# Optimization experiments

Hardware: AMD Instinct MI355X
Metric: run time of the kernel (lower is better)

Reference implementation:

```python
import jax, jax.numpy as jnp
import numpy as np

B, S, D = 2, 2048, 1024
H, DH = 16, 64  # n_heads, d_head = d_model // n_heads


def setup_inputs() -> dict:
    key = jax.random.key(0)
    ks = jax.random.split(key, 8)
    sc = lambda d: 1.0 / np.sqrt(d)
    return {
        "x": jax.random.normal(ks[0], (B, S, D), jnp.float32),
        "context": jax.random.normal(ks[1], (B, D), jnp.float32),
        "prev_state": jax.random.normal(ks[2], (B, S, D), jnp.float32),
        "attention_mask": jnp.ones((B, 1, S, S), dtype=bool),
        "Wq": jax.random.normal(ks[3], (D, D), jnp.float32) * sc(D),
        "Wk": jax.random.normal(ks[4], (D, D), jnp.float32) * sc(D),
        "Wv": jax.random.normal(ks[5], (D, D), jnp.float32) * sc(D),
        "Wo": jax.random.normal(ks[6], (D, D), jnp.float32) * sc(D),
        "Wc": jax.random.normal(ks[7], (D, DH), jnp.float32) * sc(D),
        "alpha": jnp.ones((1,), jnp.float32),
        "beta": jnp.ones((1,), jnp.float32),
    }


def reference(x, context, prev_state, attention_mask, Wq, Wk, Wv, Wo, Wc, alpha, beta):
    b, s, d = x.shape
    # projections (Linear with no bias, weight stored as [out, in] -> x @ W.T)
    q = (x @ Wq.T).reshape(b, s, H, DH).transpose(0, 2, 1, 3)  # (B,H,S,DH)
    k = (x @ Wk.T).reshape(b, s, H, DH).transpose(0, 2, 1, 3)
    v = (x @ Wv.T).reshape(b, s, H, DH).transpose(0, 2, 1, 3)

    inv_sqrt_dh = 1.0 / jnp.sqrt(jnp.asarray(DH, x.dtype))
    scores = jnp.einsum("bhqd,bhkd->bhqk", q, k) * inv_sqrt_dh

    # CFM: context-flow matching bias, rank-1 per-pair term from global context
    c = context @ Wc  # (B, DH)
    qc = jnp.einsum("bhqd,bd->bhq", q, c)
    kc = jnp.einsum("bhkd,bd->bhk", k, c)
    cfm = qc[..., :, None] * kc[..., None, :] / DH  # (B,H,S,S)

    # AFM: anti-flow matching bias from previous layer state (first d_head dims)
    p = prev_state[..., :DH]  # (B,S,DH)
    afm = jnp.einsum("bhqd,bkd->bhqk", q, p) * inv_sqrt_dh

    scores = scores + alpha[0] * cfm - beta[0] * afm
    scores = jnp.where(attention_mask, scores, jnp.asarray(-1e9, scores.dtype))

    w = jax.nn.softmax(scores, axis=-1)
    out = jnp.einsum("bhqk,bhkd->bhqd", w, v)  # (B,H,S,DH)
    out = out.transpose(0, 2, 1, 3).reshape(b, s, d)
    return out @ Wo.T
```

## Files before the change

kernel.cpp:

```cpp
#include <hip/hip_runtime.h>
#include <stdint.h>

#define D_  1024
#define S_  2048
#define B_  2
#define H_  16
#define DH_ 64
#define M_  (B_*S_)

typedef __bf16 bf16x8 __attribute__((ext_vector_type(8)));
typedef float  f32x4  __attribute__((ext_vector_type(4)));
typedef float  f32x16 __attribute__((ext_vector_type(16)));
typedef short  short8 __attribute__((ext_vector_type(8)));
typedef unsigned uint4v __attribute__((ext_vector_type(4)));
typedef unsigned short u16;

static __device__ __forceinline__ u16 f2bf(float f){
  union { float f; unsigned u; } v; v.f = f;
  unsigned r = v.u + 0x7FFF + ((v.u >> 16) & 1);
  return (u16)(r >> 16);
}
static __device__ __forceinline__ f32x4 mfma16(short8 a, short8 b, f32x4 c){
  return __builtin_amdgcn_mfma_f32_16x16x32_bf16(
      __builtin_bit_cast(bf16x8, a), __builtin_bit_cast(bf16x8, b), c, 0, 0, 0);
}
static __device__ __forceinline__ f32x16 mfma32(short8 a, short8 b, f32x16 c){
  return __builtin_amdgcn_mfma_f32_32x32x16_bf16(
      __builtin_bit_cast(bf16x8, a), __builtin_bit_cast(bf16x8, b), c, 0, 0, 0);
}
static __device__ __forceinline__ f32x16 zero16(){
  f32x16 z = {0,0,0,0,0,0,0,0,0,0,0,0,0,0,0,0};
  return z;
}
static __device__ __forceinline__ float fexp2(float x){
#if __has_builtin(__builtin_amdgcn_exp2f)
  return __builtin_amdgcn_exp2f(x);
#else
  return __exp2f(x);
#endif
}
static __device__ __forceinline__ unsigned cvtpk(float lo, float hi){
  unsigned r;
  asm("v_cvt_pk_bf16_f32 %0, %1, %2" : "=v"(r) : "v"(lo), "v"(hi));
  return r;
}
static __device__ __forceinline__ void gl_lds16(const u16* g, u16* lds){
  __builtin_amdgcn_global_load_lds(
      (const __attribute__((address_space(1))) void*)(uintptr_t)g,
      (__attribute__((address_space(3))) void*)(uintptr_t)lds, 16, 0, 0);
}

__global__ void k_f2bf(const float* __restrict__ in, u16* __restrict__ out, int n4){
  int i = blockIdx.x * blockDim.x + threadIdx.x;
  if(i >= n4) return;
  float4 v = ((const float4*)in)[i];
  ushort4 o; o.x = f2bf(v.x); o.y = f2bf(v.y); o.z = f2bf(v.z); o.w = f2bf(v.w);
  ((ushort4*)out)[i] = o;
}

__global__ void k_f2bf4(const float* __restrict__ a0, const float* __restrict__ a1,
                        const float* __restrict__ a2, const float* __restrict__ a3,
                        u16* __restrict__ o0, u16* __restrict__ o1,
                        u16* __restrict__ o2, u16* __restrict__ o3, int n4){
  const float* in; u16* out;
  switch(blockIdx.y){
    case 0: in=a0; out=o0; break;
    case 1: in=a1; out=o1; break;
    case 2: in=a2; out=o2; break;
    default: in=a3; out=o3; break;
  }
  int i = blockIdx.x * blockDim.x + threadIdx.x;
  if(i >= n4) return;
  float4 v = ((const float4*)in)[i];
  ushort4 o; o.x = f2bf(v.x); o.y = f2bf(v.y); o.z = f2bf(v.z); o.w = f2bf(v.w);
  ((ushort4*)out)[i] = o;
}

__global__ void k_ctx(const float* __restrict__ context, const float* __restrict__ Wc,
                      float* __restrict__ cvec, int* __restrict__ flags){
  __shared__ float partial[4][2][64];
  int t = threadIdx.x;
  if(t < 2) flags[t] = 1;
  int c = t >> 7;
  int b = (t >> 6) & 1;
  int j = t & 63;
  float s = 0.f;
  #pragma unroll 8
  for(int d = c*256; d < (c+1)*256; ++d) s += context[b*D_ + d] * Wc[d*DH_ + j];
  partial[c][b][j] = s;
  __syncthreads();
  if(t < 128){
    int b2 = t >> 6, j2 = t & 63;
    cvec[b2*DH_ + j2] = partial[0][b2][j2] + partial[1][b2][j2]
                      + partial[2][b2][j2] + partial[3][b2][j2];
  }
}

__global__ void k_mask_check(const uint4* __restrict__ m, int n16, int* flags){
  int i = blockIdx.x * blockDim.x + threadIdx.x;
  bool ok8 = true, ok32 = true;
  if(i < n16){
    uint4 v = m[i];
    ok8  = (v.x==0x01010101u)&&(v.y==0x01010101u)&&(v.z==0x01010101u)&&(v.w==0x01010101u);
    ok32 = (v.x==1u)&&(v.y==1u)&&(v.z==1u)&&(v.w==1u);
  }
  unsigned long long b8  = __ballot(!ok8);
  unsigned long long b32 = __ballot(!ok32);
  if((threadIdx.x & 63) == 0){
    if(b8)  flags[0] = 0;
    if(b32) flags[1] = 0;
  }
}

template<int MODE>
__global__ __launch_bounds__(256,2) void k_gemm(const u16* __restrict__ A, const u16* __restrict__ W,
                                                void* __restrict__ Cout,
                                                const float* __restrict__ cvec,
                                                const float* __restrict__ prev,
                                                const float* __restrict__ beta_p,
                                                float* __restrict__ qkc){
  __shared__ u16 As[128*64];
  __shared__ u16 Bs[64*64];
  __shared__ float red[2][2][64];
  const int tid = threadIdx.x;
  const int w = tid >> 6, l = tid & 63;
  const int wr = w >> 1, wc = w & 1;
  const int bm = blockIdx.x >> 4;
  const int bn = blockIdx.x & 15;
  const int lr = l & 15, lh = l >> 4;
  const int srow = l >> 3, scol = (l & 7) * 8;

  f32x4 acc[4][2] = {};

  for(int kt = 0; kt < 16; ++kt){
    const int k0 = kt * 64;
    #pragma unroll
    for(int i = 0; i < 4; ++i){
      const int chunk = i*4 + w;
      const u16* ga = A + (size_t)(bm*128 + chunk*8 + srow)*D_ + k0 + scol;
      gl_lds16(ga, &As[chunk*512]);
    }
    #pragma unroll
    for(int i = 0; i < 2; ++i){
      const int chunk = w*2 + i;
      const u16* gb = W + (size_t)(bn*64 + chunk*8 + srow)*D_ + k0 + scol;
      gl_lds16(gb, &Bs[chunk*512]);
    }
    __syncthreads();
    #pragma unroll
    for(int kk = 0; kk < 2; ++kk){
      short8 a[4], b[2];
      #pragma unroll
      for(int m = 0; m < 4; ++m)
        a[m] = *(const short8*)&As[(wr*64 + m*16 + lr)*64 + kk*32 + lh*8];
      #pragma unroll
      for(int n = 0; n < 2; ++n)
        b[n] = *(const short8*)&Bs[(wc*32 + n*16 + lr)*64 + kk*32 + lh*8];
      #pragma unroll
      for(int m = 0; m < 4; ++m)
        #pragma unroll
        for(int n = 0; n < 2; ++n)
          acc[m][n] = mfma16(a[m], b[n], acc[m][n]);
    }
    __syncthreads();
  }

  const int b = bm >> 4;

  if constexpr (MODE <= 1){
    const float cv0 = cvec[b*DH_ + wc*32 + lr];
    const float cv1 = cvec[b*DH_ + wc*32 + 16 + lr];
    float part[4][4];
    #pragma unroll
    for(int m = 0; m < 4; ++m)
      #pragma unroll
      for(int r = 0; r < 4; ++r){
        float p = acc[m][0][r]*cv0 + acc[m][1][r]*cv1;
        p += __shfl_xor(p, 1, 64); p += __shfl_xor(p, 2, 64);
        p += __shfl_xor(p, 4, 64); p += __shfl_xor(p, 8, 64);
        part[m][r] = p;
      }
    if(lr == 0){
      #pragma unroll
      for(int m = 0; m < 4; ++m)
        #pragma unroll
        for(int r = 0; r < 4; ++r)
          red[wr][wc][m*16 + lh*4 + r] = part[m][r];
    }
    __syncthreads();
    if(tid < 128){
      int wr2 = tid >> 6, i = tid & 63;
      float v = red[wr2][0][i] + red[wr2][1][i];
      int s = (bm & 15)*128 + wr2*64 + i;
      qkc[((size_t)b*H_ + bn)*S_ + s] = v;
    }
  }

  if constexpr (MODE == 1){
    const float beta = beta_p[0];
    const float KSCALE = 0.125f * 1.44269504088896340736f;
    #pragma unroll
    for(int m = 0; m < 4; ++m)
      #pragma unroll
      for(int n = 0; n < 2; ++n)
        #pragma unroll
        for(int r = 0; r < 4; ++r){
          size_t row = (size_t)bm*128 + wr*64 + m*16 + lh*4 + r;
          acc[m][n][r] = (acc[m][n][r] - beta * prev[row*D_ + wc*32 + n*16 + lr]) * KSCALE;
        }
  }

  if constexpr (MODE == 2){
    #pragma unroll
    for(int m = 0; m < 4; ++m){
      const int s0 = (bm & 15)*128 + wr*64 + m*16 + lh*4;
      #pragma unroll
      for(int n = 0; n < 2; ++n){
        const int col = bn*64 + wc*32 + n*16 + lr;
        ushort4 o;
        o.x = f2bf(acc[m][n][0]); o.y = f2bf(acc[m][n][1]);
        o.z = f2bf(acc[m][n][2]); o.w = f2bf(acc[m][n][3]);
        *(ushort4*)&((u16*)Cout)[((size_t)(b*1024 + col))*S_ + s0] = o;
      }
    }
  } else {
    #pragma unroll
    for(int m = 0; m < 4; ++m){
      const size_t row0 = (size_t)bm*128 + wr*64 + m*16 + lh*4;
      #pragma unroll
      for(int n = 0; n < 2; ++n){
        const size_t col = (size_t)bn*64 + wc*32 + n*16 + lr;
        #pragma unroll
        for(int r = 0; r < 4; ++r){
          if constexpr (MODE == 3) ((float*)Cout)[(row0 + r)*D_ + col] = acc[m][n][r];
          else                     ((u16*)Cout)[(row0 + r)*D_ + col] = f2bf(acc[m][n][r]);
        }
      }
    }
  }
}

__global__ __launch_bounds__(128,2) void k_attn(const u16* __restrict__ Qb,
    const u16* __restrict__ Kb, const u16* __restrict__ VT,
    const float* __restrict__ qc, const float* __restrict__ kc,
    const float* __restrict__ alpha_p, const unsigned char* __restrict__ mask,
    const int* __restrict__ flags, u16* __restrict__ Ob){
  __shared__ u16 Kbuf[2][4096];
  __shared__ u16 Vbuf[2][4096];
  const int tid = threadIdx.x;
  const int wv = tid >> 6, l = tid & 63;
  const int q32 = l & 31, hi = l >> 5, hb = hi*8;
  const int id = blockIdx.x;
  const int bh = id & 31, qb = id >> 5;
  const int b = bh >> 4, h = bh & 15;
  const int q0w = qb*64 + wv*32;
  const float aL = alpha_p[0] * (1.0f/64.0f) * 1.44269504088896340736f;
  const bool allones = (flags[0] | flags[1]) != 0;
  const u16* Kb_h = Kb + (size_t)b*S_*D_ + h*DH_;
  const u16* VT_h = VT + ((size_t)(b*1024 + h*DH_))*S_;
  const float* kcp = kc + (size_t)bh*S_;
  const unsigned char* maskr = mask + ((size_t)b*S_ + q0w + q32)*S_;

  const int srow = l >> 3;
  const int sdh  = ((l & 7) ^ srow) * 8;
  #define STAGEK(TILE, BUF) { _Pragma("unroll") for(int j = 0; j < 4; ++j){      \
      const int ck = j*2 + wv;                                                   \
      gl_lds16(Kb_h + (size_t)((TILE)*64 + ck*8 + srow)*D_ + sdh,                \
               &Kbuf[BUF][ck*512]); } }
  #define STAGEV(TILE, BUF) { _Pragma("unroll") for(int j = 0; j < 4; ++j){      \
      const int ck = j*2 + wv;                                                   \
      gl_lds16(VT_h + (size_t)(ck*8 + srow)*S_ + (TILE)*64 + sdh,                \
               &Vbuf[BUF][ck*512]); } }

  short8 qa[4];
  #pragma unroll
  for(int c = 0; c < 4; ++c)
    qa[c] = *(const short8*)&Qb[((size_t)b*S_ + q0w + q32)*D_ + h*DH_ + c*16 + hb];
  const float aq = aL * qc[(size_t)bh*S_ + q0w + q32];

  f32x16 oacc[2] = {zero16(), zero16()};
  float lp = 0.f;
  const int xk = (q32 & 7) << 3;

  STAGEK(0, 0);
  STAGEV(0, 0);
  __syncthreads();

  for(int kt = 0; kt < 32; ++kt){
    const int buf = kt & 1;
    const int k0 = kt*64;
    const int tn = (kt+1) & 31;
    STAGEK(tn, buf^1);
    STAGEV(tn, buf^1);

    f32x16 sacc[2] = {zero16(), zero16()};
    #pragma unroll
    for(int kg = 0; kg < 2; ++kg)
      #pragma unroll
      for(int c = 0; c < 4; ++c){
        short8 kf = *(const short8*)&Kbuf[buf][(kg*32 + q32)*64 + ((c*16 + hb) ^ xk)];
        sacc[kg] = mfma32(kf, qa[c], sacc[kg]);
      }
    short8 vf[2][4];
    #pragma unroll
    for(int dh2 = 0; dh2 < 2; ++dh2)
      #pragma unroll
      for(int c = 0; c < 4; ++c)
        vf[dh2][c] = *(const short8*)&Vbuf[buf][(dh2*32 + q32)*64 + ((c*16 + hb) ^ xk)];

    unsigned pk[2][8];
    #pragma unroll
    for(int kg = 0; kg < 2; ++kg){
      float p[16];
      #pragma unroll
      for(int rg = 0; rg < 4; ++rg){
        f32x4 kv = *(const f32x4*)&kcp[k0 + kg*32 + rg*8 + hi*4];
        unsigned mu = 0x01010101u;
        if(!allones) mu = *(const unsigned*)&maskr[k0 + kg*32 + rg*8 + hi*4];
        #pragma unroll
        for(int j = 0; j < 4; ++j){
          float t = sacc[kg][rg*4 + j] + aq*kv[j];
          if(((mu >> (8*j)) & 255u) == 0u) t = -160.0f;
          float e = fexp2(t);
          lp += e;
          p[rg*4 + j] = e;
        }
      }
      #pragma unroll
      for(int i = 0; i < 8; ++i) pk[kg][i] = cvtpk(p[2*i], p[2*i+1]);
    }

    #pragma unroll
    for(int c = 0; c < 4; ++c){
      const int kg = c >> 1, c4 = (c & 1)*4;
      unsigned x0 = pk[kg][c4+0], y0 = pk[kg][c4+2];
      unsigned x1 = pk[kg][c4+1], y1 = pk[kg][c4+3];
      asm("v_permlane32_swap_b32 %0, %1" : "+v"(x0), "+v"(y0));
      asm("v_permlane32_swap_b32 %0, %1" : "+v"(x1), "+v"(y1));
      uint4v pb = {x0, x1, y0, y1};
      short8 pbf = __builtin_bit_cast(short8, pb);
      #pragma unroll
      for(int dh2 = 0; dh2 < 2; ++dh2)
        oacc[dh2] = mfma32(vf[dh2][c], pbf, oacc[dh2]);
    }
    __syncthreads();
  }
  #undef STAGEK
  #undef STAGEV

  float lt = lp + __shfl_xor(lp, 32, 64);
  float inv = 1.0f / lt;
  u16* orow = Ob + ((size_t)b*S_ + q0w + q32)*D_ + h*DH_;
  #pragma unroll
  for(int dh2 = 0; dh2 < 2; ++dh2)
    #pragma unroll
    for(int rg = 0; rg < 4; ++rg){
      ushort4 o;
      o.x = f2bf(oacc[dh2][rg*4+0]*inv);
      o.y = f2bf(oacc[dh2][rg*4+1]*inv);
      o.z = f2bf(oacc[dh2][rg*4+2]*inv);
      o.w = f2bf(oacc[dh2][rg*4+3]*inv);
      *(ushort4*)&orow[dh2*32 + rg*8 + hi*4] = o;
    }
}

extern "C" void kernel_launch(void* const* d_in, const int* in_sizes, int n_in,
                              void* d_out, int out_size, void* d_ws, size_t ws_size,
                              hipStream_t stream){
  const float* x    = (const float*)d_in[0];
  const float* ctx  = (const float*)d_in[1];
  const float* prev = (const float*)d_in[2];
  const unsigned char* mask = (const unsigned char*)d_in[3];
  const float* Wq = (const float*)d_in[4];
  const float* Wk = (const float*)d_in[5];
  const float* Wv = (const float*)d_in[6];
  const float* Wo = (const float*)d_in[7];
  const float* Wc = (const float*)d_in[8];
  const float* alpha = (const float*)d_in[9];
  const float* beta  = (const float*)d_in[10];

  char* ws = (char*)d_ws;
  size_t off = 0;
  auto alloc = [&](size_t bytes)->void*{
    void* p = ws + off; off += (bytes + 255) & ~(size_t)255; return p;
  };
  u16* xb  = (u16*)alloc((size_t)M_*D_*2);
  u16* wqb = (u16*)alloc((size_t)D_*D_*2);
  u16* wkb = (u16*)alloc((size_t)D_*D_*2);
  u16* wvb = (u16*)alloc((size_t)D_*D_*2);
  u16* wob = (u16*)alloc((size_t)D_*D_*2);
  u16* Qb  = (u16*)alloc((size_t)M_*D_*2);
  u16* Kb  = (u16*)alloc((size_t)M_*D_*2);
  u16* VT  = (u16*)alloc((size_t)B_*D_*S_*2);
  float* qcb  = (float*)alloc((size_t)B_*H_*S_*4);
  float* kcb  = (float*)alloc((size_t)B_*H_*S_*4);
  float* cvec = (float*)alloc(512);
  int*  flags = (int*)alloc(64);
  u16* Ob = xb;

  k_f2bf<<<M_*D_/4/256, 256, 0, stream>>>(x, xb, M_*D_/4);
  {
    dim3 g(D_*D_/4/256, 4);
    k_f2bf4<<<g, 256, 0, stream>>>(Wq, Wk, Wv, Wo, wqb, wkb, wvb, wob, D_*D_/4);
  }
  k_ctx<<<1, 512, 0, stream>>>(ctx, Wc, cvec, flags);
  {
    int n16 = B_*S_*S_/16;
    k_mask_check<<<n16/256, 256, 0, stream>>>((const uint4*)mask, n16, flags);
  }
  k_gemm<0><<<512, 256, 0, stream>>>(xb, wqb, Qb, cvec, nullptr, nullptr, qcb);
  k_gemm<1><<<512, 256, 0, stream>>>(xb, wkb, Kb, cvec, prev, beta, kcb);
  k_gemm<2><<<512, 256, 0, stream>>>(xb, wvb, VT, cvec, nullptr, nullptr, nullptr);
  k_attn<<<1024, 128, 0, stream>>>(Qb, Kb, VT, qcb, kcb, alpha, mask, flags, Ob);
  k_gemm<3><<<512, 256, 0, stream>>>(Ob, wob, d_out, cvec, nullptr, nullptr, nullptr);
}
```

Before: 174.2 us.

## Split attention KV range across warps and enlarge GEMM tiles to 128x128

The GEMM kernels move from 128x64 to 128x128 output tiles (256 blocks, launch bounds of 1), which doubles per-wave MFMA work and reuse of the A tile. Attention now uses 256 threads per block, with two warp pairs each covering half the key range; partial outputs and row sums are combined through LDS at the end. V fragments are read straight from global memory instead of being staged in LDS. The all-ones mask path becomes a template specialization. Risks are fewer GEMM blocks on a large GPU (only 256 tiles), uncoalesced or uncached global V reads, and extra LDS reduction cost.

```diff
diff --git a/kernel.cpp b/kernel.cpp
--- a/kernel.cpp
+++ b/kernel.cpp
@@ -113,53 +113,47 @@
 }
 
 template<int MODE>
-__global__ __launch_bounds__(256,2) void k_gemm(const u16* __restrict__ A, const u16* __restrict__ W,
+__global__ __launch_bounds__(256,1) void k_gemm(const u16* __restrict__ A, const u16* __restrict__ W,
                                                 void* __restrict__ Cout,
                                                 const float* __restrict__ cvec,
                                                 const float* __restrict__ prev,
                                                 const float* __restrict__ beta_p,
                                                 float* __restrict__ qkc){
   __shared__ u16 As[128*64];
-  __shared__ u16 Bs[64*64];
+  __shared__ u16 Bs[128*64];
   __shared__ float red[2][2][64];
   const int tid = threadIdx.x;
   const int w = tid >> 6, l = tid & 63;
   const int wr = w >> 1, wc = w & 1;
-  const int bm = blockIdx.x >> 4;
-  const int bn = blockIdx.x & 15;
+  const int bm = blockIdx.x >> 3;
+  const int bn = blockIdx.x & 7;
   const int lr = l & 15, lh = l >> 4;
   const int srow = l >> 3, scol = (l & 7) * 8;
 
-  f32x4 acc[4][2] = {};
+  f32x4 acc[4][4] = {};
 
   for(int kt = 0; kt < 16; ++kt){
     const int k0 = kt * 64;
     #pragma unroll
     for(int i = 0; i < 4; ++i){
       const int chunk = i*4 + w;
-      const u16* ga = A + (size_t)(bm*128 + chunk*8 + srow)*D_ + k0 + scol;
-      gl_lds16(ga, &As[chunk*512]);
-    }
-    #pragma unroll
-    for(int i = 0; i < 2; ++i){
-      const int chunk = w*2 + i;
-      const u16* gb = W + (size_t)(bn*64 + chunk*8 + srow)*D_ + k0 + scol;
-      gl_lds16(gb, &Bs[chunk*512]);
+      gl_lds16(A + (size_t)(bm*128 + chunk*8 + srow)*D_ + k0 + scol, &As[chunk*512]);
+      gl_lds16(W + (size_t)(bn*128 + chunk*8 + srow)*D_ + k0 + scol, &Bs[chunk*512]);
     }
     __syncthreads();
     #pragma unroll
     for(int kk = 0; kk < 2; ++kk){
-      short8 a[4], b[2];
+      short8 a[4], b[4];
       #pragma unroll
       for(int m = 0; m < 4; ++m)
         a[m] = *(const short8*)&As[(wr*64 + m*16 + lr)*64 + kk*32 + lh*8];
       #pragma unroll
-      for(int n = 0; n < 2; ++n)
-        b[n] = *(const short8*)&Bs[(wc*32 + n*16 + lr)*64 + kk*32 + lh*8];
+      for(int n = 0; n < 4; ++n)
+        b[n] = *(const short8*)&Bs[(wc*64 + n*16 + lr)*64 + kk*32 + lh*8];
       #pragma unroll
       for(int m = 0; m < 4; ++m)
         #pragma unroll
-        for(int n = 0; n < 2; ++n)
+        for(int n = 0; n < 4; ++n)
           acc[m][n] = mfma16(a[m], b[n], acc[m][n]);
     }
     __syncthreads();
@@ -168,14 +162,16 @@
   const int b = bm >> 4;
 
   if constexpr (MODE <= 1){
-    const float cv0 = cvec[b*DH_ + wc*32 + lr];
-    const float cv1 = cvec[b*DH_ + wc*32 + 16 + lr];
+    float cv[4];
+    #pragma unroll
+    for(int n = 0; n < 4; ++n) cv[n] = cvec[b*DH_ + n*16 + lr];
     float part[4][4];
     #pragma unroll
     for(int m = 0; m < 4; ++m)
       #pragma unroll
       for(int r = 0; r < 4; ++r){
-        float p = acc[m][0][r]*cv0 + acc[m][1][r]*cv1;
+        float p = acc[m][0][r]*cv[0] + acc[m][1][r]*cv[1]
+                + acc[m][2][r]*cv[2] + acc[m][3][r]*cv[3];
         p += __shfl_xor(p, 1, 64); p += __shfl_xor(p, 2, 64);
         p += __shfl_xor(p, 4, 64); p += __shfl_xor(p, 8, 64);
         part[m][r] = p;
@@ -188,11 +184,10 @@
           red[wr][wc][m*16 + lh*4 + r] = part[m][r];
     }
     __syncthreads();
-    if(tid < 128){
-      int wr2 = tid >> 6, i = tid & 63;
-      float v = red[wr2][0][i] + red[wr2][1][i];
+    {
+      int wr2 = tid >> 7, wc2 = (tid >> 6) & 1, i = tid & 63;
       int s = (bm & 15)*128 + wr2*64 + i;
-      qkc[((size_t)b*H_ + bn)*S_ + s] = v;
+      qkc[((size_t)b*H_ + bn*2 + wc2)*S_ + s] = red[wr2][wc2][i];
     }
   }
 
@@ -202,11 +197,11 @@
     #pragma unroll
     for(int m = 0; m < 4; ++m)
       #pragma unroll
-      for(int n = 0; n < 2; ++n)
+      for(int n = 0; n < 4; ++n)
         #pragma unroll
         for(int r = 0; r < 4; ++r){
           size_t row = (size_t)bm*128 + wr*64 + m*16 + lh*4 + r;
-          acc[m][n][r] = (acc[m][n][r] - beta * prev[row*D_ + wc*32 + n*16 + lr]) * KSCALE;
+          acc[m][n][r] = (acc[m][n][r] - beta * prev[row*D_ + n*16 + lr]) * KSCALE;
         }
   }
 
@@ -215,8 +210,8 @@
     for(int m = 0; m < 4; ++m){
       const int s0 = (bm & 15)*128 + wr*64 + m*16 + lh*4;
       #pragma unroll
-      for(int n = 0; n < 2; ++n){
-        const int col = bn*64 + wc*32 + n*16 + lr;
+      for(int n = 0; n < 4; ++n){
+        const int col = bn*128 + wc*64 + n*16 + lr;
         ushort4 o;
         o.x = f2bf(acc[m][n][0]); o.y = f2bf(acc[m][n][1]);
         o.z = f2bf(acc[m][n][2]); o.w = f2bf(acc[m][n][3]);
@@ -228,8 +223,8 @@
     for(int m = 0; m < 4; ++m){
       const size_t row0 = (size_t)bm*128 + wr*64 + m*16 + lh*4;
       #pragma unroll
-      for(int n = 0; n < 2; ++n){
-        const size_t col = (size_t)bn*64 + wc*32 + n*16 + lr;
+      for(int n = 0; n < 4; ++n){
+        const size_t col = (size_t)bn*128 + wc*64 + n*16 + lr;
         #pragma unroll
         for(int r = 0; r < 4; ++r){
           if constexpr (MODE == 3) ((float*)Cout)[(row0 + r)*D_ + col] = acc[m][n][r];
@@ -240,74 +235,38 @@
   }
 }
 
-__global__ __launch_bounds__(128,2) void k_attn(const u16* __restrict__ Qb,
-    const u16* __restrict__ Kb, const u16* __restrict__ VT,
-    const float* __restrict__ qc, const float* __restrict__ kc,
-    const float* __restrict__ alpha_p, const unsigned char* __restrict__ mask,
-    const int* __restrict__ flags, u16* __restrict__ Ob){
-  __shared__ u16 Kbuf[2][4096];
-  __shared__ u16 Vbuf[2][4096];
-  const int tid = threadIdx.x;
-  const int wv = tid >> 6, l = tid & 63;
-  const int q32 = l & 31, hi = l >> 5, hb = hi*8;
-  const int id = blockIdx.x;
-  const int bh = id & 31, qb = id >> 5;
-  const int b = bh >> 4, h = bh & 15;
-  const int q0w = qb*64 + wv*32;
-  const float aL = alpha_p[0] * (1.0f/64.0f) * 1.44269504088896340736f;
-  const bool allones = (flags[0] | flags[1]) != 0;
-  const u16* Kb_h = Kb + (size_t)b*S_*D_ + h*DH_;
-  const u16* VT_h = VT + ((size_t)(b*1024 + h*DH_))*S_;
-  const float* kcp = kc + (size_t)bh*S_;
-  const unsigned char* maskr = mask + ((size_t)b*S_ + q0w + q32)*S_;
-
-  const int srow = l >> 3;
-  const int sdh  = ((l & 7) ^ srow) * 8;
-  #define STAGEK(TILE, BUF) { _Pragma("unroll") for(int j = 0; j < 4; ++j){      \
-      const int ck = j*2 + wv;                                                   \
-      gl_lds16(Kb_h + (size_t)((TILE)*64 + ck*8 + srow)*D_ + sdh,                \
-               &Kbuf[BUF][ck*512]); } }
-  #define STAGEV(TILE, BUF) { _Pragma("unroll") for(int j = 0; j < 4; ++j){      \
-      const int ck = j*2 + wv;                                                   \
-      gl_lds16(VT_h + (size_t)(ck*8 + srow)*S_ + (TILE)*64 + sdh,                \
-               &Vbuf[BUF][ck*512]); } }
-
-  short8 qa[4];
-  #pragma unroll
-  for(int c = 0; c < 4; ++c)
-    qa[c] = *(const short8*)&Qb[((size_t)b*S_ + q0w + q32)*D_ + h*DH_ + c*16 + hb];
-  const float aq = aL * qc[(size_t)bh*S_ + q0w + q32];
-
-  f32x16 oacc[2] = {zero16(), zero16()};
-  float lp = 0.f;
-  const int xk = (q32 & 7) << 3;
-
-  STAGEK(0, 0);
-  STAGEV(0, 0);
+template<bool AM>
+__device__ __forceinline__ void attn_loop(
+    const u16* __restrict__ Kstream, const u16* __restrict__ VTk,
+    const float* __restrict__ kcp, const unsigned char* __restrict__ maskr,
+    u16* __restrict__ kbuf, const short8 (&qa)[4], float aq,
+    f32x16 (&oacc)[2], float& lp,
+    int q32, int hi, int hb, int srow, int sdh, int stg0, int xk){
+  #define STG(T, BUF) { _Pragma("unroll") for(int j = 0; j < 4; ++j){            \
+      const int ck = stg0 + j;                                                   \
+      gl_lds16(Kstream + (size_t)((T)*64 + ck*8 + srow)*D_ + sdh,                \
+               kbuf + (BUF)*4096 + ck*512); } }
+  STG(0, 0);
   __syncthreads();
-
-  for(int kt = 0; kt < 32; ++kt){
-    const int buf = kt & 1;
-    const int k0 = kt*64;
-    const int tn = (kt+1) & 31;
-    STAGEK(tn, buf^1);
-    STAGEV(tn, buf^1);
-
+  #pragma unroll 2
+  for(int t = 0; t < 16; ++t){
+    const int buf = t & 1;
+    const int k0 = t*64;
+    if(t < 15) STG(t+1, buf^1);
+    short8 vf[2][4];
+    #pragma unroll
+    for(int dh2 = 0; dh2 < 2; ++dh2)
+      #pragma unroll
+      for(int c = 0; c < 4; ++c)
+        vf[dh2][c] = *(const short8*)&VTk[(size_t)(dh2*32 + q32)*S_ + k0 + c*16 + hb];
     f32x16 sacc[2] = {zero16(), zero16()};
     #pragma unroll
     for(int kg = 0; kg < 2; ++kg)
       #pragma unroll
       for(int c = 0; c < 4; ++c){
-        short8 kf = *(const short8*)&Kbuf[buf][(kg*32 + q32)*64 + ((c*16 + hb) ^ xk)];
+        short8 kf = *(const short8*)&kbuf[buf*4096 + (kg*32 + q32)*64 + ((c*16 + hb) ^ xk)];
         sacc[kg] = mfma32(kf, qa[c], sacc[kg]);
       }
-    short8 vf[2][4];
-    #pragma unroll
-    for(int dh2 = 0; dh2 < 2; ++dh2)
-      #pragma unroll
-      for(int c = 0; c < 4; ++c)
-        vf[dh2][c] = *(const short8*)&Vbuf[buf][(dh2*32 + q32)*64 + ((c*16 + hb) ^ xk)];
-
     unsigned pk[2][8];
     #pragma unroll
     for(int kg = 0; kg < 2; ++kg){
@@ -316,12 +275,12 @@
       for(int rg = 0; rg < 4; ++rg){
         f32x4 kv = *(const f32x4*)&kcp[k0 + kg*32 + rg*8 + hi*4];
         unsigned mu = 0x01010101u;
-        if(!allones) mu = *(const unsigned*)&maskr[k0 + kg*32 + rg*8 + hi*4];
+        if(AM) mu = *(const unsigned*)&maskr[k0 + kg*32 + rg*8 + hi*4];
         #pragma unroll
         for(int j = 0; j < 4; ++j){
-          float t = sacc[kg][rg*4 + j] + aq*kv[j];
-          if(((mu >> (8*j)) & 255u) == 0u) t = -160.0f;
-          float e = fexp2(t);
+          float tv = sacc[kg][rg*4 + j] + aq*kv[j];
+          if(AM){ if(((mu >> (8*j)) & 255u) == 0u) tv = -160.0f; }
+          float e = fexp2(tv);
           lp += e;
           p[rg*4 + j] = e;
         }
@@ -329,7 +288,6 @@
       #pragma unroll
       for(int i = 0; i < 8; ++i) pk[kg][i] = cvtpk(p[2*i], p[2*i+1]);
     }
-
     #pragma unroll
     for(int c = 0; c < 4; ++c){
       const int kg = c >> 1, c4 = (c & 1)*4;
@@ -345,23 +303,77 @@
     }
     __syncthreads();
   }
-  #undef STAGEK
-  #undef STAGEV
-
-  float lt = lp + __shfl_xor(lp, 32, 64);
-  float inv = 1.0f / lt;
-  u16* orow = Ob + ((size_t)b*S_ + q0w + q32)*D_ + h*DH_;
+  #undef STG
+}
+
+__global__ __launch_bounds__(256,2) void k_attn(const u16* __restrict__ Qb,
+    const u16* __restrict__ Kb, const u16* __restrict__ VT,
+    const float* __restrict__ qc, const float* __restrict__ kc,
+    const float* __restrict__ alpha_p, const unsigned char* __restrict__ mask,
+    const int* __restrict__ flags, u16* __restrict__ Ob){
+  __shared__ u16 Kbuf[2][2][4096];
+  const int tid = threadIdx.x;
+  const int w = tid >> 6, l = tid & 63;
+  const int qi = w & 1, kh = w >> 1;
+  const int q32 = l & 31, hi = l >> 5, hb = hi*8;
+  const int id = blockIdx.x;
+  const int bh = id & 31, qb = id >> 5;
+  const int b = bh >> 4, h = bh & 15;
+  const int q0w = qb*64 + qi*32;
+  const float aL = alpha_p[0] * (1.0f/64.0f) * 1.44269504088896340736f;
+  const bool allones = (flags[0] | flags[1]) != 0;
+  const u16* Kstream = Kb + (size_t)b*S_*D_ + h*DH_ + (size_t)kh*1024*D_;
+  const u16* VTk = VT + ((size_t)(b*1024 + h*DH_))*S_ + kh*1024;
+  const float* kcp = kc + (size_t)bh*S_ + kh*1024;
+  const unsigned char* maskr = mask + ((size_t)b*S_ + q0w + q32)*S_ + kh*1024;
+  const int srow = l >> 3;
+  const int sdh  = ((l & 7) ^ srow) * 8;
+  const int stg0 = qi*4;
+  const int xk   = (q32 & 7) << 3;
+
+  short8 qa[4];
   #pragma unroll
-  for(int dh2 = 0; dh2 < 2; ++dh2)
-    #pragma unroll
-    for(int rg = 0; rg < 4; ++rg){
-      ushort4 o;
-      o.x = f2bf(oacc[dh2][rg*4+0]*inv);
-      o.y = f2bf(oacc[dh2][rg*4+1]*inv);
-      o.z = f2bf(oacc[dh2][rg*4+2]*inv);
-      o.w = f2bf(oacc[dh2][rg*4+3]*inv);
-      *(ushort4*)&orow[dh2*32 + rg*8 + hi*4] = o;
-    }
+  for(int c = 0; c < 4; ++c)
+    qa[c] = *(const short8*)&Qb[((size_t)b*S_ + q0w + q32)*D_ + h*DH_ + c*16 + hb];
+  const float aq = aL * qc[(size_t)bh*S_ + q0w + q32];
+
+  f32x16 oacc[2] = {zero16(), zero16()};
+  float lp = 0.f;
+
+  if(allones)
+    attn_loop<false>(Kstream, VTk, kcp, maskr, &Kbuf[kh][0][0], qa, aq,
+                     oacc, lp, q32, hi, hb, srow, sdh, stg0, xk);
+  else
+    attn_loop<true>(Kstream, VTk, kcp, maskr, &Kbuf[kh][0][0], qa, aq,
+                    oacc, lp, q32, hi, hb, srow, sdh, stg0, xk);
+
+  float* C = (float*)&Kbuf[0][0][0];
+  float* R = C + qi*2112;
+  if(kh == 1){
+    #pragma unroll
+    for(int i = 0; i < 32; ++i) R[i*64 + l] = oacc[i>>4][i&15];
+    R[2048 + l] = lp;
+  }
+  __syncthreads();
+  if(kh == 0){
+    #pragma unroll
+    for(int i = 0; i < 32; ++i) oacc[i>>4][i&15] += R[i*64 + l];
+    lp += R[2048 + l];
+    float lt = lp + __shfl_xor(lp, 32, 64);
+    float inv = 1.0f / lt;
+    u16* orow = Ob + ((size_t)b*S_ + q0w + q32)*D_ + h*DH_;
+    #pragma unroll
+    for(int dh2 = 0; dh2 < 2; ++dh2)
+      #pragma unroll
+      for(int rg = 0; rg < 4; ++rg){
+        ushort4 o;
+        o.x = f2bf(oacc[dh2][rg*4+0]*inv);
+        o.y = f2bf(oacc[dh2][rg*4+1]*inv);
+        o.z = f2bf(oacc[dh2][rg*4+2]*inv);
+        o.w = f2bf(oacc[dh2][rg*4+3]*inv);
+        *(ushort4*)&orow[dh2*32 + rg*8 + hi*4] = o;
+      }
+  }
 }
 
 extern "C" void kernel_launch(void* const* d_in, const int* in_sizes, int n_in,
@@ -408,9 +420,9 @@
     int n16 = B_*S_*S_/16;
     k_mask_check<<<n16/256, 256, 0, stream>>>((const uint4*)mask, n16, flags);
   }
-  k_gemm<0><<<512, 256, 0, stream>>>(xb, wqb, Qb, cvec, nullptr, nullptr, qcb);
-  k_gemm<1><<<512, 256, 0, stream>>>(xb, wkb, Kb, cvec, prev, beta, kcb);
-  k_gemm<2><<<512, 256, 0, stream>>>(xb, wvb, VT, cvec, nullptr, nullptr, nullptr);
-  k_attn<<<1024, 128, 0, stream>>>(Qb, Kb, VT, qcb, kcb, alpha, mask, flags, Ob);
-  k_gemm<3><<<512, 256, 0, stream>>>(Ob, wob, d_out, cvec, nullptr, nullptr, nullptr);
-}
+  k_gemm<0><<<256, 256, 0, stream>>>(xb, wqb, Qb, cvec, nullptr, nullptr, qcb);
+  k_gemm<1><<<256, 256, 0, stream>>>(xb, wkb, Kb, cvec, prev, beta, kcb);
+  k_gemm<2><<<256, 256, 0, stream>>>(xb, wvb, VT, cvec, nullptr, nullptr, nullptr);
+  k_attn<<<1024, 256, 0, stream>>>(Qb, Kb, VT, qcb, kcb, alpha, mask, flags, Ob);
+  k_gemm<3><<<256, 256, 0, stream>>>(Ob, wob, d_out, cvec, nullptr, nullptr, nullptr);
+}
```

Measured after the change: 229.3 us. 31.7% more time.

## Fuse Q/K/V projections into one GEMM with concatenated weights and wider tiles

Applied to the files above, without the earlier changes.

Concatenates Wq, Wk and Wv into a single bf16 weight buffer and replaces three separate projection GEMM launches with one 768-block kernel using 128x128 output tiles. The per-tile epilogue then branches on column block to write Q plus qc, K plus kc with the prev-state correction, or transposed V. This removes two launches, fills the GPU with a single larger grid, and doubles the B-tile reuse of each A tile. In exchange, each thread holds more accumulator registers, which may reduce occupancy, and the epilogue has divergent per-block paths.

```diff
diff --git a/kernel.cpp b/kernel.cpp
--- a/kernel.cpp
+++ b/kernel.cpp
@@ -112,16 +112,134 @@
   }
 }
 
-template<int MODE>
-__global__ __launch_bounds__(256,2) void k_gemm(const u16* __restrict__ A, const u16* __restrict__ W,
-                                                void* __restrict__ Cout,
-                                                const float* __restrict__ cvec,
-                                                const float* __restrict__ prev,
-                                                const float* __restrict__ beta_p,
-                                                float* __restrict__ qkc){
+__global__ __launch_bounds__(256,2) void k_gemm_qkv(const u16* __restrict__ A,
+    const u16* __restrict__ Wcat, u16* __restrict__ Qb, u16* __restrict__ Kb,
+    u16* __restrict__ VT, const float* __restrict__ cvec,
+    const float* __restrict__ prev, const float* __restrict__ beta_p,
+    float* __restrict__ qcb, float* __restrict__ kcb){
+  __shared__ u16 As[128*64];
+  __shared__ u16 Bs[128*64];
+  __shared__ float red[2][2][64];
+  const int tid = threadIdx.x;
+  const int w = tid >> 6, l = tid & 63;
+  const int wr = w >> 1, wc = w & 1;
+  const int id = blockIdx.x;
+  const int bn = id >> 5;
+  const int bm = id & 31;
+  const int lr = l & 15, lh = l >> 4;
+  const int srow = l >> 3, scol = (l & 7) * 8;
+
+  f32x4 acc[4][4] = {};
+
+  for(int kt = 0; kt < 16; ++kt){
+    const int k0 = kt * 64;
+    #pragma unroll
+    for(int i = 0; i < 4; ++i){
+      const int chunk = i*4 + w;
+      gl_lds16(A    + (size_t)(bm*128 + chunk*8 + srow)*D_ + k0 + scol, &As[chunk*512]);
+      gl_lds16(Wcat + (size_t)(bn*128 + chunk*8 + srow)*D_ + k0 + scol, &Bs[chunk*512]);
+    }
+    __syncthreads();
+    #pragma unroll
+    for(int kk = 0; kk < 2; ++kk){
+      short8 a[4], b[4];
+      #pragma unroll
+      for(int m = 0; m < 4; ++m)
+        a[m] = *(const short8*)&As[(wr*64 + m*16 + lr)*64 + kk*32 + lh*8];
+      #pragma unroll
+      for(int n = 0; n < 4; ++n)
+        b[n] = *(const short8*)&Bs[(wc*64 + n*16 + lr)*64 + kk*32 + lh*8];
+      #pragma unroll
+      for(int m = 0; m < 4; ++m)
+        #pragma unroll
+        for(int n = 0; n < 4; ++n)
+          acc[m][n] = mfma16(a[m], b[n], acc[m][n]);
+    }
+    __syncthreads();
+  }
+
+  const int b = bm >> 4;
+
+  if(bn < 16){
+    float cv[4];
+    #pragma unroll
+    for(int n = 0; n < 4; ++n) cv[n] = cvec[b*DH_ + n*16 + lr];
+    float part[4][4];
+    #pragma unroll
+    for(int m = 0; m < 4; ++m)
+      #pragma unroll
+      for(int r = 0; r < 4; ++r){
+        float p = acc[m][0][r]*cv[0] + acc[m][1][r]*cv[1]
+                + acc[m][2][r]*cv[2] + acc[m][3][r]*cv[3];
+        p += __shfl_xor(p, 1, 64); p += __shfl_xor(p, 2, 64);
+        p += __shfl_xor(p, 4, 64); p += __shfl_xor(p, 8, 64);
+        part[m][r] = p;
+      }
+    if(lr == 0){
+      #pragma unroll
+      for(int m = 0; m < 4; ++m)
+        #pragma unroll
+        for(int r = 0; r < 4; ++r)
+          red[wr][wc][m*16 + lh*4 + r] = part[m][r];
+    }
+    __syncthreads();
+    {
+      int wr2 = tid >> 7, wc2 = (tid >> 6) & 1, i = tid & 63;
+      int s = (bm & 15)*128 + wr2*64 + i;
+      int head = (bn & 7)*2 + wc2;
+      float* qkc = (bn < 8) ? qcb : kcb;
+      qkc[((size_t)b*H_ + head)*S_ + s] = red[wr2][wc2][i];
+    }
+  }
+
+  if(bn < 8){
+    #pragma unroll
+    for(int m = 0; m < 4; ++m){
+      const size_t row0 = (size_t)bm*128 + wr*64 + m*16 + lh*4;
+      #pragma unroll
+      for(int n = 0; n < 4; ++n){
+        const size_t col = (size_t)bn*128 + wc*64 + n*16 + lr;
+        #pragma unroll
+        for(int r = 0; r < 4; ++r)
+          Qb[(row0 + r)*D_ + col] = f2bf(acc[m][n][r]);
+      }
+    }
+  } else if(bn < 16){
+    const float beta = beta_p[0];
+    const float KSCALE = 0.125f * 1.44269504088896340736f;
+    #pragma unroll
+    for(int m = 0; m < 4; ++m){
+      const size_t row0 = (size_t)bm*128 + wr*64 + m*16 + lh*4;
+      #pragma unroll
+      for(int n = 0; n < 4; ++n){
+        const size_t col = (size_t)(bn - 8)*128 + wc*64 + n*16 + lr;
+        #pragma unroll
+        for(int r = 0; r < 4; ++r){
+          float v = (acc[m][n][r] - beta * prev[(row0 + r)*D_ + n*16 + lr]) * KSCALE;
+          Kb[(row0 + r)*D_ + col] = f2bf(v);
+        }
+      }
+    }
+  } else {
+    #pragma unroll
+    for(int m = 0; m < 4; ++m){
+      const int s0 = (bm & 15)*128 + wr*64 + m*16 + lh*4;
+      #pragma unroll
+      for(int n = 0; n < 4; ++n){
+        const int col = (bn - 16)*128 + wc*64 + n*16 + lr;
+        ushort4 o;
+        o.x = f2bf(acc[m][n][0]); o.y = f2bf(acc[m][n][1]);
+        o.z = f2bf(acc[m][n][2]); o.w = f2bf(acc[m][n][3]);
+        *(ushort4*)&VT[((size_t)(b*1024 + col))*S_ + s0] = o;
+      }
+    }
+  }
+}
+
+__global__ __launch_bounds__(256,2) void k_gemm_o(const u16* __restrict__ A,
+    const u16* __restrict__ W, float* __restrict__ Cout){
   __shared__ u16 As[128*64];
   __shared__ u16 Bs[64*64];
-  __shared__ float red[2][2][64];
   const int tid = threadIdx.x;
   const int w = tid >> 6, l = tid & 63;
   const int wr = w >> 1, wc = w & 1;
@@ -137,14 +255,12 @@
     #pragma unroll
     for(int i = 0; i < 4; ++i){
       const int chunk = i*4 + w;
-      const u16* ga = A + (size_t)(bm*128 + chunk*8 + srow)*D_ + k0 + scol;
-      gl_lds16(ga, &As[chunk*512]);
+      gl_lds16(A + (size_t)(bm*128 + chunk*8 + srow)*D_ + k0 + scol, &As[chunk*512]);
     }
     #pragma unroll
     for(int i = 0; i < 2; ++i){
       const int chunk = w*2 + i;
-      const u16* gb = W + (size_t)(bn*64 + chunk*8 + srow)*D_ + k0 + scol;
-      gl_lds16(gb, &Bs[chunk*512]);
+      gl_lds16(W + (size_t)(bn*64 + chunk*8 + srow)*D_ + k0 + scol, &Bs[chunk*512]);
     }
     __syncthreads();
     #pragma unroll
@@ -164,78 +280,15 @@
     }
     __syncthreads();
   }
-
-  const int b = bm >> 4;
-
-  if constexpr (MODE <= 1){
-    const float cv0 = cvec[b*DH_ + wc*32 + lr];
-    const float cv1 = cvec[b*DH_ + wc*32 + 16 + lr];
-    float part[4][4];
-    #pragma unroll
-    for(int m = 0; m < 4; ++m)
-      #pragma unroll
-      for(int r = 0; r < 4; ++r){
-        float p = acc[m][0][r]*cv0 + acc[m][1][r]*cv1;
-        p += __shfl_xor(p, 1, 64); p += __shfl_xor(p, 2, 64);
-        p += __shfl_xor(p, 4, 64); p += __shfl_xor(p, 8, 64);
-        part[m][r] = p;
-      }
-    if(lr == 0){
-      #pragma unroll
-      for(int m = 0; m < 4; ++m)
-        #pragma unroll
-        for(int r = 0; r < 4; ++r)
-          red[wr][wc][m*16 + lh*4 + r] = part[m][r];
-    }
-    __syncthreads();
-    if(tid < 128){
-      int wr2 = tid >> 6, i = tid & 63;
-      float v = red[wr2][0][i] + red[wr2][1][i];
-      int s = (bm & 15)*128 + wr2*64 + i;
-      qkc[((size_t)b*H_ + bn)*S_ + s] = v;
-    }
-  }
-
-  if constexpr (MODE == 1){
-    const float beta = beta_p[0];
-    const float KSCALE = 0.125f * 1.44269504088896340736f;
-    #pragma unroll
-    for(int m = 0; m < 4; ++m)
-      #pragma unroll
-      for(int n = 0; n < 2; ++n)
-        #pragma unroll
-        for(int r = 0; r < 4; ++r){
-          size_t row = (size_t)bm*128 + wr*64 + m*16 + lh*4 + r;
-          acc[m][n][r] = (acc[m][n][r] - beta * prev[row*D_ + wc*32 + n*16 + lr]) * KSCALE;
-        }
-  }
-
-  if constexpr (MODE == 2){
-    #pragma unroll
-    for(int m = 0; m < 4; ++m){
-      const int s0 = (bm & 15)*128 + wr*64 + m*16 + lh*4;
-      #pragma unroll
-      for(int n = 0; n < 2; ++n){
-        const int col = bn*64 + wc*32 + n*16 + lr;
-        ushort4 o;
-        o.x = f2bf(acc[m][n][0]); o.y = f2bf(acc[m][n][1]);
-        o.z = f2bf(acc[m][n][2]); o.w = f2bf(acc[m][n][3]);
-        *(ushort4*)&((u16*)Cout)[((size_t)(b*1024 + col))*S_ + s0] = o;
-      }
-    }
-  } else {
-    #pragma unroll
-    for(int m = 0; m < 4; ++m){
-      const size_t row0 = (size_t)bm*128 + wr*64 + m*16 + lh*4;
-      #pragma unroll
-      for(int n = 0; n < 2; ++n){
-        const size_t col = (size_t)bn*64 + wc*32 + n*16 + lr;
-        #pragma unroll
-        for(int r = 0; r < 4; ++r){
-          if constexpr (MODE == 3) ((float*)Cout)[(row0 + r)*D_ + col] = acc[m][n][r];
-          else                     ((u16*)Cout)[(row0 + r)*D_ + col] = f2bf(acc[m][n][r]);
-        }
-      }
+  #pragma unroll
+  for(int m = 0; m < 4; ++m){
+    const size_t row0 = (size_t)bm*128 + wr*64 + m*16 + lh*4;
+    #pragma unroll
+    for(int n = 0; n < 2; ++n){
+      const size_t col = (size_t)bn*64 + wc*32 + n*16 + lr;
+      #pragma unroll
+      for(int r = 0; r < 4; ++r)
+        Cout[(row0 + r)*D_ + col] = acc[m][n][r];
     }
   }
 }
@@ -384,14 +437,12 @@
   auto alloc = [&](size_t bytes)->void*{
     void* p = ws + off; off += (bytes + 255) & ~(size_t)255; return p;
   };
-  u16* xb  = (u16*)alloc((size_t)M_*D_*2);
-  u16* wqb = (u16*)alloc((size_t)D_*D_*2);
-  u16* wkb = (u16*)alloc((size_t)D_*D_*2);
-  u16* wvb = (u16*)alloc((size_t)D_*D_*2);
-  u16* wob = (u16*)alloc((size_t)D_*D_*2);
-  u16* Qb  = (u16*)alloc((size_t)M_*D_*2);
-  u16* Kb  = (u16*)alloc((size_t)M_*D_*2);
-  u16* VT  = (u16*)alloc((size_t)B_*D_*S_*2);
+  u16* xb   = (u16*)alloc((size_t)M_*D_*2);
+  u16* wcat = (u16*)alloc((size_t)3*D_*D_*2);
+  u16* wob  = (u16*)alloc((size_t)D_*D_*2);
+  u16* Qb   = (u16*)alloc((size_t)M_*D_*2);
+  u16* Kb   = (u16*)alloc((size_t)M_*D_*2);
+  u16* VT   = (u16*)alloc((size_t)B_*D_*S_*2);
   float* qcb  = (float*)alloc((size_t)B_*H_*S_*4);
   float* kcb  = (float*)alloc((size_t)B_*H_*S_*4);
   float* cvec = (float*)alloc(512);
@@ -401,16 +452,15 @@
   k_f2bf<<<M_*D_/4/256, 256, 0, stream>>>(x, xb, M_*D_/4);
   {
     dim3 g(D_*D_/4/256, 4);
-    k_f2bf4<<<g, 256, 0, stream>>>(Wq, Wk, Wv, Wo, wqb, wkb, wvb, wob, D_*D_/4);
+    k_f2bf4<<<g, 256, 0, stream>>>(Wq, Wk, Wv, Wo,
+        wcat, wcat + (size_t)D_*D_, wcat + (size_t)2*D_*D_, wob, D_*D_/4);
   }
   k_ctx<<<1, 512, 0, stream>>>(ctx, Wc, cvec, flags);
   {
     int n16 = B_*S_*S_/16;
     k_mask_check<<<n16/256, 256, 0, stream>>>((const uint4*)mask, n16, flags);
   }
-  k_gemm<0><<<512, 256, 0, stream>>>(xb, wqb, Qb, cvec, nullptr, nullptr, qcb);
-  k_gemm<1><<<512, 256, 0, stream>>>(xb, wkb, Kb, cvec, prev, beta, kcb);
-  k_gemm<2><<<512, 256, 0, stream>>>(xb, wvb, VT, cvec, nullptr, nullptr, nullptr);
+  k_gemm_qkv<<<768, 256, 0, stream>>>(xb, wcat, Qb, Kb, VT, cvec, prev, beta, qcb, kcb);
   k_attn<<<1024, 128, 0, stream>>>(Qb, Kb, VT, qcb, kcb, alpha, mask, flags, Ob);
-  k_gemm<3><<<512, 256, 0, stream>>>(Ob, wob, d_out, cvec, nullptr, nullptr, nullptr);
-}
+  k_gemm_o<<<512, 256, 0, stream>>>(Ob, wob, (float*)d_out);
+}
```

After: 147.4 us, median of 2. -15.3%, faster.
